# Optimization experiments

Hardware: AMD Instinct MI355X
Metric: run time of the kernel (lower is better)

The kernel has to match this reference:

```python
import jax, jax.numpy as jnp
import numpy as np
from jax import lax

DM, DS, K, EXPAND = 512, 16, 4, 1
DI = EXPAND * DM           # d_inner
DT_RANK = (DM + 15) // 16  # ceil(d_model/16) = 32
B, L = 4, 2048


def setup_inputs() -> dict:
    key = jax.random.key(0)
    ks = jax.random.split(key, 10)
    x = jax.random.normal(ks[0], (B, L, DM), dtype=jnp.float32)
    W_in = jax.random.normal(ks[1], (2 * DI, DM), dtype=jnp.float32) * (1.0 / np.sqrt(DM))
    conv_w = jax.random.normal(ks[2], (DI, 1, K), dtype=jnp.float32) * (1.0 / np.sqrt(K))
    conv_b = jax.random.normal(ks[3], (DI,), dtype=jnp.float32) * 0.02
    W_xproj = jax.random.normal(ks[4], (DT_RANK + 2 * DS, DI), dtype=jnp.float32) * (1.0 / np.sqrt(DI))
    W_dt = jax.random.normal(ks[5], (DI, DT_RANK), dtype=jnp.float32) * (1.0 / np.sqrt(DT_RANK))
    b_dt = jax.random.uniform(ks[6], (DI,), dtype=jnp.float32, minval=-4.0, maxval=-2.0)  # softplus(b)~small dt
    A_log = jnp.log(jnp.broadcast_to(jnp.arange(1, DS + 1, dtype=jnp.float32), (DI, DS)))
    D_param = jnp.ones((DI,), dtype=jnp.float32)
    W_out = jax.random.normal(ks[7], (DM, DI), dtype=jnp.float32) * (1.0 / np.sqrt(DI))
    return {"x": x, "W_in": W_in, "conv_w": conv_w, "conv_b": conv_b,
            "W_xproj": W_xproj, "W_dt": W_dt, "b_dt": b_dt,
            "A_log": A_log, "D_param": D_param, "W_out": W_out}


def _mamba(x, W_in, conv_w, conv_b, W_xproj, W_dt, b_dt, A_log, D_param, W_out):
    # in_proj -> x, z branches [B,L,DI] each
    xz = jnp.einsum('bld,ed->ble', x, W_in)
    xc, z = xz[..., :DI], xz[..., DI:]
    # causal depthwise conv1d over time
    xt = jnp.transpose(xc, (0, 2, 1))                      # [B,DI,L]
    xt = jnp.pad(xt, ((0, 0), (0, 0), (K - 1, 0)))
    xt = lax.conv_general_dilated(xt, conv_w, (1,), 'VALID',
                                  dimension_numbers=('NCH', 'OIH', 'NCH'),
                                  feature_group_count=DI)
    xt = xt + conv_b[None, :, None]
    xc = jax.nn.silu(jnp.transpose(xt, (0, 2, 1)))         # [B,L,DI]
    # input-dependent dt, B, C
    x_dbl = jnp.einsum('bld,ed->ble', xc, W_xproj)         # [B,L,DT_RANK+2*DS]
    dt = x_dbl[..., :DT_RANK]
    Bm = x_dbl[..., DT_RANK:DT_RANK + DS]                  # [B,L,DS]
    Cm = x_dbl[..., DT_RANK + DS:]                         # [B,L,DS]
    dt = jax.nn.softplus(jnp.einsum('blr,dr->bld', dt, W_dt) + b_dt)  # [B,L,DI]
    A = -jnp.exp(A_log)                                    # [DI,DS]
    deltaA = jnp.exp(dt[..., None] * A)                    # [B,L,DI,DS]
    deltaBu = dt[..., None] * Bm[:, :, None, :] * xc[..., None]       # [B,L,DI,DS]

    def step(h, inp):
        dA_t, dBu_t, C_t = inp                             # [B,DI,DS],[B,DI,DS],[B,DS]
        h = dA_t * h + dBu_t
        y = jnp.einsum('bds,bs->bd', h, C_t)
        return h, y

    h0 = jnp.zeros((x.shape[0], DI, DS), dtype=x.dtype)
    _, ys = lax.scan(step, h0, (jnp.transpose(deltaA, (1, 0, 2, 3)),
                                jnp.transpose(deltaBu, (1, 0, 2, 3)),
                                jnp.transpose(Cm, (1, 0, 2))))
    y = jnp.transpose(ys, (1, 0, 2)) + xc * D_param        # [B,L,DI]
    y = y * jax.nn.silu(z)
    out = jnp.einsum('bld,ed->ble', y, W_out)              # [B,L,DM]
    out = jnp.clip(out, -1000.0, 1000.0)
    out = jnp.nan_to_num(out, nan=0.0, posinf=1000.0, neginf=-1000.0)
    return out


def reference(x, W_in, conv_w, conv_b, W_xproj, W_dt, b_dt, A_log, D_param, W_out):
    return _mamba(x, W_in, conv_w, conv_b, W_xproj, W_dt, b_dt, A_log, D_param, W_out)
```

## Files before the change

kernel.cpp:

```cpp
#include <hip/hip_runtime.h>
#include <math.h>

#define DMc   512
#define DIc   512
#define DSc   16
#define KCc   4
#define DTRc  32
#define NXDc  64
#define LLEN  2048
#define BBc   4
#define BLT   (BBc*LLEN)

#define NCH   128
#define CLEN  (LLEN/NCH)

typedef __attribute__((ext_vector_type(8))) short short8;
typedef __attribute__((ext_vector_type(8))) unsigned short ushort8;
typedef __attribute__((ext_vector_type(4))) float f32x4;

__device__ __forceinline__ float sigmoidf_(float x) { return 1.f / (1.f + __expf(-x)); }

__device__ __forceinline__ unsigned short f2bf(float x) {
    unsigned int u = __float_as_uint(x);
    u = (u + 0x7FFFu + ((u >> 16) & 1u)) >> 16;
    return (unsigned short)u;
}

#define CN1 (BLT * DMc / 8)
#define CN2 (1024 * DMc / 8)
#define CN3 (DMc * DIc / 8)
__global__ __launch_bounds__(256) void convert3_kernel(const float* __restrict__ x,
                                                       const float* __restrict__ Win,
                                                       const float* __restrict__ Wout,
                                                       unsigned short* __restrict__ xb,
                                                       unsigned short* __restrict__ Wb,
                                                       unsigned short* __restrict__ Wob)
{
    int i = blockIdx.x * 256 + threadIdx.x;
    const float* src; unsigned short* dst;
    if (i < CN1)                  { src = x;    dst = xb;  }
    else if (i < CN1 + CN2)       { src = Win;  dst = Wb;  i -= CN1; }
    else if (i < CN1 + CN2 + CN3) { src = Wout; dst = Wob; i -= CN1 + CN2; }
    else return;
    float4 a = ((const float4*)src)[2 * i];
    float4 b = ((const float4*)src)[2 * i + 1];
    ushort8 o;
    o[0] = f2bf(a.x); o[1] = f2bf(a.y); o[2] = f2bf(a.z); o[3] = f2bf(a.w);
    o[4] = f2bf(b.x); o[5] = f2bf(b.y); o[6] = f2bf(b.z); o[7] = f2bf(b.w);
    ((ushort8*)dst)[i] = o;
}

template<int EPI>
__global__ __launch_bounds__(256) void gemm_bt_f32(const float* __restrict__ A,
                                                   const float* __restrict__ Bw,
                                                   const float* __restrict__ bias,
                                                   float* __restrict__ C,
                                                   int M, int N, int Kd,
                                                   int lda, int ldb, int ldc)
{
    __shared__ float As[16][68];
    __shared__ float Bs[16][68];
    const int tid  = threadIdx.x;
    const int tx   = tid & 15;
    const int ty   = tid >> 4;
    const int arow = tid >> 2;
    const int akq  = (tid & 3) << 2;

    const float* Ab = A  + (size_t)(blockIdx.y * 64 + arow) * lda + akq;
    const float* Bb = Bw + (size_t)(blockIdx.x * 64 + arow) * ldb + akq;

    float acc[4][4] = {};

    for (int k0 = 0; k0 < Kd; k0 += 16) {
        float4 av = *(const float4*)(Ab + k0);
        float4 bv = *(const float4*)(Bb + k0);
        __syncthreads();
        As[akq + 0][arow] = av.x; As[akq + 1][arow] = av.y;
        As[akq + 2][arow] = av.z; As[akq + 3][arow] = av.w;
        Bs[akq + 0][arow] = bv.x; Bs[akq + 1][arow] = bv.y;
        Bs[akq + 2][arow] = bv.z; Bs[akq + 3][arow] = bv.w;
        __syncthreads();
#pragma unroll
        for (int k = 0; k < 16; ++k) {
            float4 a = *(const float4*)&As[k][ty << 2];
            float4 b = *(const float4*)&Bs[k][tx << 2];
            float ar[4] = {a.x, a.y, a.z, a.w};
            float br[4] = {b.x, b.y, b.z, b.w};
#pragma unroll
            for (int i = 0; i < 4; ++i)
#pragma unroll
                for (int j = 0; j < 4; ++j)
                    acc[i][j] += ar[i] * br[j];
        }
    }

    float4 bv = make_float4(0.f, 0.f, 0.f, 0.f);
    if (EPI == 2) bv = *(const float4*)(bias + blockIdx.x * 64 + (tx << 2));
#pragma unroll
    for (int i = 0; i < 4; ++i) {
        float v[4] = {acc[i][0], acc[i][1], acc[i][2], acc[i][3]};
        if (EPI == 2) {
            float bb[4] = {bv.x, bv.y, bv.z, bv.w};
#pragma unroll
            for (int j = 0; j < 4; ++j) {
                float s = v[j] + bb[j];
                v[j] = fmaxf(s, 0.f) + log1pf(__expf(-fabsf(s)));
            }
        }
        *(float4*)(C + (size_t)(blockIdx.y * 64 + (ty << 2) + i) * ldc
                     + blockIdx.x * 64 + (tx << 2)) = make_float4(v[0], v[1], v[2], v[3]);
    }
}

template<int EPI>
__global__ __launch_bounds__(256) void gemm_mfma(const unsigned short* __restrict__ A,
                                                 const unsigned short* __restrict__ Bw,
                                                 float* __restrict__ C,
                                                 int M, int N, int Kd)
{
    __shared__ short As[128][40];
    __shared__ short Bs[128][40];
    const int tid  = threadIdx.x;
    const int lane = tid & 63;
    const int wv   = tid >> 6;
    const int wr   = wv >> 1;
    const int wc   = wv & 1;
    const int fr   = lane & 15;
    const int fq   = lane >> 4;

    const int rowA0 = blockIdx.y * 128;
    const int rowB0 = blockIdx.x * 128;

    const int r0 = tid >> 2,        s0 = (tid & 3) << 3;
    const int r1 = (tid + 256) >> 2, s1 = s0;

    f32x4 acc[4][4];
#pragma unroll
    for (int m = 0; m < 4; ++m)
#pragma unroll
        for (int n = 0; n < 4; ++n) acc[m][n] = (f32x4){0.f, 0.f, 0.f, 0.f};

    for (int k0 = 0; k0 < Kd; k0 += 32) {
        short8 a0 = *(const short8*)(A  + (size_t)(rowA0 + r0) * Kd + k0 + s0);
        short8 a1 = *(const short8*)(A  + (size_t)(rowA0 + r1) * Kd + k0 + s1);
        short8 b0 = *(const short8*)(Bw + (size_t)(rowB0 + r0) * Kd + k0 + s0);
        short8 b1 = *(const short8*)(Bw + (size_t)(rowB0 + r1) * Kd + k0 + s1);
        __syncthreads();
        *(short8*)&As[r0][s0] = a0;
        *(short8*)&As[r1][s1] = a1;
        *(short8*)&Bs[r0][s0] = b0;
        *(short8*)&Bs[r1][s1] = b1;
        __syncthreads();

        short8 af[4], bf[4];
#pragma unroll
        for (int m = 0; m < 4; ++m)
            af[m] = *(const short8*)&As[wr * 64 + m * 16 + fr][fq << 3];
#pragma unroll
        for (int n = 0; n < 4; ++n)
            bf[n] = *(const short8*)&Bs[wc * 64 + n * 16 + fr][fq << 3];
#pragma unroll
        for (int m = 0; m < 4; ++m)
#pragma unroll
            for (int n = 0; n < 4; ++n)
                acc[m][n] = __builtin_amdgcn_mfma_f32_16x16x32_bf16(af[m], bf[n], acc[m][n], 0, 0, 0);
    }

    const int crow0 = rowA0 + wr * 64 + (fq << 2);
    const int ccol0 = rowB0 + wc * 64 + fr;
#pragma unroll
    for (int m = 0; m < 4; ++m)
#pragma unroll
        for (int n = 0; n < 4; ++n)
#pragma unroll
            for (int j = 0; j < 4; ++j) {
                float v = acc[m][n][j];
                if (EPI) v = (v != v) ? 0.f : fminf(fmaxf(v, -1000.f), 1000.f);
                C[(size_t)(crow0 + m * 16 + j) * N + ccol0 + n * 16] = v;
            }
}

__global__ __launch_bounds__(256) void conv_silu_kernel(const float* __restrict__ xz,
                                                        const float* __restrict__ cw,
                                                        const float* __restrict__ cb,
                                                        float* __restrict__ xc)
{
    int gid = blockIdx.x * 256 + threadIdx.x;
    int d = gid & (DIc - 1);
    int l = (gid >> 9) & (LLEN - 1);
    int b = gid >> 20;
    float s = cb[d];
#pragma unroll
    for (int k = 0; k < KCc; ++k) {
        int ls = l + k - (KCc - 1);
        if (ls >= 0)
            s += xz[((size_t)(b * LLEN + ls) << 10) + d] * cw[d * KCc + k];
    }
    xc[gid] = s * sigmoidf_(s);
}

__device__ __forceinline__ size_t hs_off(int b, int c, int s, int d) {
    return ((size_t)((b * NCH + c) * DSc + s) << 9) + d;
}

__global__ __launch_bounds__(256) void scan_phase1(const float* __restrict__ dtz,
                                                   const float* __restrict__ xc,
                                                   const float* __restrict__ xdbl,
                                                   const float* __restrict__ A_log,
                                                   float* __restrict__ hstate,
                                                   float* __restrict__ sdtbuf)
{
    int half = blockIdx.x & 1;
    int c    = (blockIdx.x >> 1) & (NCH - 1);
    int b    = blockIdx.x >> 8;
    int d    = (half << 8) + threadIdx.x;
    int row0 = b * LLEN + c * CLEN;

    __shared__ float bc[CLEN][32];
    {
        int r = threadIdx.x >> 4, col = (threadIdx.x & 15) << 1;
        const float* src = xdbl + (size_t)(row0 + r) * NXDc + DTRc + col;
        bc[r][col] = src[0]; bc[r][col + 1] = src[1];
    }

    float A[DSc];
#pragma unroll
    for (int s = 0; s < DSc; ++s) A[s] = -__expf(A_log[d * DSc + s]);

    float dtv[CLEN], xcv[CLEN];
#pragma unroll
    for (int t = 0; t < CLEN; ++t) {
        dtv[t] = dtz[((size_t)(row0 + t) << 10) + d];
        xcv[t] = xc [((size_t)(row0 + t) << 9) + d];
    }
    __syncthreads();

    float h[DSc] = {};
    float Sdt = 0.f;
#pragma unroll
    for (int t = 0; t < CLEN; ++t) {
        float dBx = dtv[t] * xcv[t];
        Sdt += dtv[t];
#pragma unroll
        for (int s = 0; s < DSc; ++s)
            h[s] = __expf(dtv[t] * A[s]) * h[s] + dBx * bc[t][s];
    }
#pragma unroll
    for (int s = 0; s < DSc; ++s) hstate[hs_off(b, c, s, d)] = h[s];
    sdtbuf[((size_t)(b * NCH + c) << 9) + d] = Sdt;
}

__global__ __launch_bounds__(64) void scan_phase2(float* __restrict__ hstate,
                                                  const float* __restrict__ sdtbuf,
                                                  const float* __restrict__ A_log)
{
    int gid = blockIdx.x * 64 + threadIdx.x;
    int d = gid & (DIc - 1);
    int s = (gid >> 9) & (DSc - 1);
    int b = gid >> 13;

    float A = -__expf(A_log[d * DSc + s]);
    float h = 0.f;
    for (int c = 0; c < NCH; ++c) {
        size_t o = hs_off(b, c, s, d);
        float he  = hstate[o];
        float Sdt = sdtbuf[((size_t)(b * NCH + c) << 9) + d];
        hstate[o] = h;
        h = __expf(A * Sdt) * h + he;
    }
}

__global__ __launch_bounds__(256) void scan_phase3(const float* __restrict__ dtz,
                                                   const float* __restrict__ xc,
                                                   const float* __restrict__ xdbl,
                                                   const float* __restrict__ hstate,
                                                   const float* __restrict__ A_log,
                                                   const float* __restrict__ Dp,
                                                   unsigned short* __restrict__ yb)
{
    int half = blockIdx.x & 1;
    int c    = (blockIdx.x >> 1) & (NCH - 1);
    int b    = blockIdx.x >> 8;
    int d    = (half << 8) + threadIdx.x;
    int row0 = b * LLEN + c * CLEN;

    __shared__ float bc[CLEN][32];
    {
        int r = threadIdx.x >> 4, col = (threadIdx.x & 15) << 1;
        const float* src = xdbl + (size_t)(row0 + r) * NXDc + DTRc + col;
        bc[r][col] = src[0]; bc[r][col + 1] = src[1];
    }

    float A[DSc];
#pragma unroll
    for (int s = 0; s < DSc; ++s) A[s] = -__expf(A_log[d * DSc + s]);
    float Dv = Dp[d];

    float dtv[CLEN], xcv[CLEN], zv[CLEN];
#pragma unroll
    for (int t = 0; t < CLEN; ++t) {
        dtv[t] = dtz[((size_t)(row0 + t) << 10) + d];
        xcv[t] = xc [((size_t)(row0 + t) << 9) + d];
        zv[t]  = dtz[((size_t)(row0 + t) << 10) + DIc + d];
    }

    float h[DSc];
#pragma unroll
    for (int s = 0; s < DSc; ++s) h[s] = hstate[hs_off(b, c, s, d)];
    __syncthreads();

#pragma unroll
    for (int t = 0; t < CLEN; ++t) {
        float dBx = dtv[t] * xcv[t];
        float acc = 0.f;
#pragma unroll
        for (int s = 0; s < DSc; ++s) {
            float dA = __expf(dtv[t] * A[s]);
            h[s] = dA * h[s] + dBx * bc[t][s];
            acc += h[s] * bc[t][DSc + s];
        }
        float yv = (acc + xcv[t] * Dv) * (zv[t] * sigmoidf_(zv[t]));
        yb[((size_t)(row0 + t) << 9) + d] = f2bf(yv);
    }
}

extern "C" void kernel_launch(void* const* d_in, const int* in_sizes, int n_in,
                              void* d_out, int out_size, void* d_ws, size_t ws_size,
                              hipStream_t stream)
{
    const float* x      = (const float*)d_in[0];
    const float* W_in   = (const float*)d_in[1];
    const float* conv_w = (const float*)d_in[2];
    const float* conv_b = (const float*)d_in[3];
    const float* W_xp   = (const float*)d_in[4];
    const float* W_dt   = (const float*)d_in[5];
    const float* b_dt   = (const float*)d_in[6];
    const float* A_log  = (const float*)d_in[7];
    const float* D_par  = (const float*)d_in[8];
    const float* W_out  = (const float*)d_in[9];
    float* out = (float*)d_out;

    float* ws   = (float*)d_ws;
    float* xz   = ws;
    float* xc   = xz + (size_t)BLT * 1024;
    float* xdbl = xc + (size_t)BLT * DIc;
    unsigned short* xb  = (unsigned short*)(xdbl + (size_t)BLT * NXDc);
    unsigned short* Wb  = xb + (size_t)BLT * DIc;
    unsigned short* Wob = Wb + (size_t)1024 * DMc;
    float* hstate = (float*)(Wob + (size_t)DMc * DIc);
    float* sdtbuf = hstate + (size_t)BBc * NCH * DSc * DIc;

    convert3_kernel<<<(CN1 + CN2 + CN3 + 255) / 256, 256, 0, stream>>>(
        x, W_in, W_out, xb, Wb, Wob);

    gemm_mfma<0><<<dim3(1024 / 128, BLT / 128), 256, 0, stream>>>(xb, Wb, xz, BLT, 1024, DMc);

    conv_silu_kernel<<<(BLT * DIc) / 256, 256, 0, stream>>>(xz, conv_w, conv_b, xc);

    gemm_bt_f32<0><<<dim3(1, BLT / 64), 256, 0, stream>>>(xc, W_xp, nullptr, xdbl,
                                                          BLT, NXDc, DIc, DIc, DIc, NXDc);

    gemm_bt_f32<2><<<dim3(DIc / 64, BLT / 64), 256, 0, stream>>>(xdbl, W_dt, b_dt, xz,
                                                                 BLT, DIc, DTRc, NXDc, DTRc, 1024);

    scan_phase1<<<BBc * NCH * 2, 256, 0, stream>>>(xz, xc, xdbl, A_log, hstate, sdtbuf);
    scan_phase2<<<(BBc * DSc * DIc) / 64, 64, 0, stream>>>(hstate, sdtbuf, A_log);
    scan_phase3<<<BBc * NCH * 2, 256, 0, stream>>>(xz, xc, xdbl, hstate, A_log, D_par, xb);

    gemm_mfma<1><<<dim3(DMc / 128, BLT / 128), 256, 0, stream>>>(xb, Wob, out, BLT, DMc, DMc);
}
```

Before: 169.6 us.

## Store xz and xc intermediates in bf16 and remap GEMM workgroups

The in_proj GEMM now writes bf16 instead of fp32. The conv+SiLU kernel is vectorized to read and write bf16 in groups of 8. The x_proj GEMM gets a dedicated kernel that reads bf16 activations, and the scans read bf16 xc and z with dt kept in a separate compact fp32 buffer. This cuts intermediate memory traffic across several kernels, and a workgroup index swizzle is added to the MFMA GEMM to improve cache locality. The cost is lower precision on activations feeding the SSM scan, which could hurt accuracy.

```diff
diff --git a/kernel.cpp b/kernel.cpp
--- a/kernel.cpp
+++ b/kernel.cpp
@@ -16,6 +16,7 @@
 
 typedef __attribute__((ext_vector_type(8))) short short8;
 typedef __attribute__((ext_vector_type(8))) unsigned short ushort8;
+typedef __attribute__((ext_vector_type(4))) unsigned short bf16x4_t;
 typedef __attribute__((ext_vector_type(4))) float f32x4;
 
 __device__ __forceinline__ float sigmoidf_(float x) { return 1.f / (1.f + __expf(-x)); }
@@ -24,6 +25,9 @@
     unsigned int u = __float_as_uint(x);
     u = (u + 0x7FFFu + ((u >> 16) & 1u)) >> 16;
     return (unsigned short)u;
+}
+__device__ __forceinline__ float bf2f(unsigned short u) {
+    return __uint_as_float((unsigned int)u << 16);
 }
 
 #define CN1 (BLT * DMc / 8)
@@ -112,12 +116,65 @@
     }
 }
 
-template<int EPI>
+__global__ __launch_bounds__(256) void gemm_xdbl(const unsigned short* __restrict__ A,
+                                                 const float* __restrict__ Bw,
+                                                 float* __restrict__ C)
+{
+    __shared__ float As[16][68];
+    __shared__ float Bs[16][68];
+    const int tid  = threadIdx.x;
+    const int tx   = tid & 15;
+    const int ty   = tid >> 4;
+    const int arow = tid >> 2;
+    const int akq  = (tid & 3) << 2;
+
+    const unsigned short* Ab = A + (size_t)(blockIdx.y * 64 + arow) * DIc + akq;
+    const float*          Bb = Bw + (size_t)arow * DIc + akq;
+
+    float acc[4][4] = {};
+
+    for (int k0 = 0; k0 < DIc; k0 += 16) {
+        bf16x4_t av = *(const bf16x4_t*)(Ab + k0);
+        float4   bv = *(const float4*)(Bb + k0);
+        __syncthreads();
+        As[akq + 0][arow] = bf2f(av[0]); As[akq + 1][arow] = bf2f(av[1]);
+        As[akq + 2][arow] = bf2f(av[2]); As[akq + 3][arow] = bf2f(av[3]);
+        Bs[akq + 0][arow] = bv.x; Bs[akq + 1][arow] = bv.y;
+        Bs[akq + 2][arow] = bv.z; Bs[akq + 3][arow] = bv.w;
+        __syncthreads();
+#pragma unroll
+        for (int k = 0; k < 16; ++k) {
+            float4 a = *(const float4*)&As[k][ty << 2];
+            float4 b = *(const float4*)&Bs[k][tx << 2];
+            float ar[4] = {a.x, a.y, a.z, a.w};
+            float br[4] = {b.x, b.y, b.z, b.w};
+#pragma unroll
+            for (int i = 0; i < 4; ++i)
+#pragma unroll
+                for (int j = 0; j < 4; ++j)
+                    acc[i][j] += ar[i] * br[j];
+        }
+    }
+
+#pragma unroll
+    for (int i = 0; i < 4; ++i)
+        *(float4*)(C + (size_t)(blockIdx.y * 64 + (ty << 2) + i) * NXDc + (tx << 2))
+            = make_float4(acc[i][0], acc[i][1], acc[i][2], acc[i][3]);
+}
+
+template<int EPI, int OBF>
 __global__ __launch_bounds__(256) void gemm_mfma(const unsigned short* __restrict__ A,
                                                  const unsigned short* __restrict__ Bw,
-                                                 float* __restrict__ C,
-                                                 int M, int N, int Kd)
-{
+                                                 float* __restrict__ Cf,
+                                                 unsigned short* __restrict__ Cb,
+                                                 int N, int Kd)
+{
+    const int nwg  = gridDim.x * gridDim.y;
+    const int orig = blockIdx.y * gridDim.x + blockIdx.x;
+    const int lg   = (orig & 7) * (nwg >> 3) + (orig >> 3);
+    const int bx   = lg % gridDim.x;
+    const int by   = lg / gridDim.x;
+
     __shared__ short As[128][40];
     __shared__ short Bs[128][40];
     const int tid  = threadIdx.x;
@@ -128,8 +185,8 @@
     const int fr   = lane & 15;
     const int fq   = lane >> 4;
 
-    const int rowA0 = blockIdx.y * 128;
-    const int rowB0 = blockIdx.x * 128;
+    const int rowA0 = by * 128;
+    const int rowB0 = bx * 128;
 
     const int r0 = tid >> 2,        s0 = (tid & 3) << 3;
     const int r1 = (tid + 256) >> 2, s1 = s0;
@@ -176,27 +233,43 @@
             for (int j = 0; j < 4; ++j) {
                 float v = acc[m][n][j];
                 if (EPI) v = (v != v) ? 0.f : fminf(fmaxf(v, -1000.f), 1000.f);
-                C[(size_t)(crow0 + m * 16 + j) * N + ccol0 + n * 16] = v;
+                size_t off = (size_t)(crow0 + m * 16 + j) * N + ccol0 + n * 16;
+                if (OBF) Cb[off] = f2bf(v);
+                else     Cf[off] = v;
             }
 }
 
-__global__ __launch_bounds__(256) void conv_silu_kernel(const float* __restrict__ xz,
+__global__ __launch_bounds__(256) void conv_silu_kernel(const unsigned short* __restrict__ xzb,
                                                         const float* __restrict__ cw,
                                                         const float* __restrict__ cb,
-                                                        float* __restrict__ xc)
+                                                        unsigned short* __restrict__ xcb)
 {
     int gid = blockIdx.x * 256 + threadIdx.x;
-    int d = gid & (DIc - 1);
-    int l = (gid >> 9) & (LLEN - 1);
-    int b = gid >> 20;
-    float s = cb[d];
+    int d8 = gid & 63;
+    int l  = (gid >> 6) & (LLEN - 1);
+    int b  = gid >> 17;
+    int d0 = d8 << 3;
+
+    float s[8];
+#pragma unroll
+    for (int j = 0; j < 8; ++j) s[j] = cb[d0 + j];
 #pragma unroll
     for (int k = 0; k < KCc; ++k) {
         int ls = l + k - (KCc - 1);
-        if (ls >= 0)
-            s += xz[((size_t)(b * LLEN + ls) << 10) + d] * cw[d * KCc + k];
-    }
-    xc[gid] = s * sigmoidf_(s);
+        if (ls >= 0) {
+            ushort8 v = *(const ushort8*)(xzb + (((size_t)(b * LLEN + ls)) << 10) + d0);
+#pragma unroll
+            for (int j = 0; j < 8; ++j)
+                s[j] += bf2f(v[j]) * cw[(d0 + j) * KCc + k];
+        }
+    }
+    ushort8 o;
+#pragma unroll
+    for (int j = 0; j < 8; ++j) {
+        float v = s[j] * sigmoidf_(s[j]);
+        o[j] = f2bf(v);
+    }
+    *(ushort8*)(xcb + ((size_t)gid << 3)) = o;
 }
 
 __device__ __forceinline__ size_t hs_off(int b, int c, int s, int d) {
@@ -204,7 +277,7 @@
 }
 
 __global__ __launch_bounds__(256) void scan_phase1(const float* __restrict__ dtz,
-                                                   const float* __restrict__ xc,
+                                                   const unsigned short* __restrict__ xcb,
                                                    const float* __restrict__ xdbl,
                                                    const float* __restrict__ A_log,
                                                    float* __restrict__ hstate,
@@ -230,8 +303,8 @@
     float dtv[CLEN], xcv[CLEN];
 #pragma unroll
     for (int t = 0; t < CLEN; ++t) {
-        dtv[t] = dtz[((size_t)(row0 + t) << 10) + d];
-        xcv[t] = xc [((size_t)(row0 + t) << 9) + d];
+        dtv[t] = dtz[((size_t)(row0 + t) << 9) + d];
+        xcv[t] = bf2f(xcb[((size_t)(row0 + t) << 9) + d]);
     }
     __syncthreads();
 
@@ -271,8 +344,9 @@
 }
 
 __global__ __launch_bounds__(256) void scan_phase3(const float* __restrict__ dtz,
-                                                   const float* __restrict__ xc,
+                                                   const unsigned short* __restrict__ xcb,
                                                    const float* __restrict__ xdbl,
+                                                   const unsigned short* __restrict__ xzb,
                                                    const float* __restrict__ hstate,
                                                    const float* __restrict__ A_log,
                                                    const float* __restrict__ Dp,
@@ -299,9 +373,9 @@
     float dtv[CLEN], xcv[CLEN], zv[CLEN];
 #pragma unroll
     for (int t = 0; t < CLEN; ++t) {
-        dtv[t] = dtz[((size_t)(row0 + t) << 10) + d];
-        xcv[t] = xc [((size_t)(row0 + t) << 9) + d];
-        zv[t]  = dtz[((size_t)(row0 + t) << 10) + DIc + d];
+        dtv[t] = dtz[((size_t)(row0 + t) << 9) + d];
+        xcv[t] = bf2f(xcb[((size_t)(row0 + t) << 9) + d]);
+        zv[t]  = bf2f(xzb[((size_t)(row0 + t) << 10) + DIc + d]);
     }
 
     float h[DSc];
@@ -340,32 +414,34 @@
     const float* W_out  = (const float*)d_in[9];
     float* out = (float*)d_out;
 
-    float* ws   = (float*)d_ws;
-    float* xz   = ws;
-    float* xc   = xz + (size_t)BLT * 1024;
-    float* xdbl = xc + (size_t)BLT * DIc;
-    unsigned short* xb  = (unsigned short*)(xdbl + (size_t)BLT * NXDc);
-    unsigned short* Wb  = xb + (size_t)BLT * DIc;
-    unsigned short* Wob = Wb + (size_t)1024 * DMc;
-    float* hstate = (float*)(Wob + (size_t)DMc * DIc);
+    unsigned short* xb   = (unsigned short*)d_ws;
+    unsigned short* xzb  = xb  + (size_t)BLT * DIc;
+    unsigned short* xcb  = xzb + (size_t)BLT * 1024;
+    unsigned short* Wb   = xcb + (size_t)BLT * DIc;
+    unsigned short* Wob  = Wb  + (size_t)1024 * DMc;
+    float* xdbl   = (float*)(Wob + (size_t)DMc * DIc);
+    float* dtz    = xdbl + (size_t)BLT * NXDc;
+    float* hstate = dtz  + (size_t)BLT * DIc;
     float* sdtbuf = hstate + (size_t)BBc * NCH * DSc * DIc;
 
     convert3_kernel<<<(CN1 + CN2 + CN3 + 255) / 256, 256, 0, stream>>>(
         x, W_in, W_out, xb, Wb, Wob);
 
-    gemm_mfma<0><<<dim3(1024 / 128, BLT / 128), 256, 0, stream>>>(xb, Wb, xz, BLT, 1024, DMc);
-
-    conv_silu_kernel<<<(BLT * DIc) / 256, 256, 0, stream>>>(xz, conv_w, conv_b, xc);
-
-    gemm_bt_f32<0><<<dim3(1, BLT / 64), 256, 0, stream>>>(xc, W_xp, nullptr, xdbl,
-                                                          BLT, NXDc, DIc, DIc, DIc, NXDc);
-
-    gemm_bt_f32<2><<<dim3(DIc / 64, BLT / 64), 256, 0, stream>>>(xdbl, W_dt, b_dt, xz,
-                                                                 BLT, DIc, DTRc, NXDc, DTRc, 1024);
-
-    scan_phase1<<<BBc * NCH * 2, 256, 0, stream>>>(xz, xc, xdbl, A_log, hstate, sdtbuf);
+    gemm_mfma<0, 1><<<dim3(1024 / 128, BLT / 128), 256, 0, stream>>>(
+        xb, Wb, nullptr, xzb, 1024, DMc);
+
+    conv_silu_kernel<<<(BLT * DIc / 8) / 256, 256, 0, stream>>>(xzb, conv_w, conv_b, xcb);
+
+    gemm_xdbl<<<dim3(1, BLT / 64), 256, 0, stream>>>(xcb, W_xp, xdbl);
+
+    gemm_bt_f32<2><<<dim3(DIc / 64, BLT / 64), 256, 0, stream>>>(
+        xdbl, W_dt, b_dt, dtz, BLT, DIc, DTRc, NXDc, DTRc, DIc);
+
+    scan_phase1<<<BBc * NCH * 2, 256, 0, stream>>>(dtz, xcb, xdbl, A_log, hstate, sdtbuf);
     scan_phase2<<<(BBc * DSc * DIc) / 64, 64, 0, stream>>>(hstate, sdtbuf, A_log);
-    scan_phase3<<<BBc * NCH * 2, 256, 0, stream>>>(xz, xc, xdbl, hstate, A_log, D_par, xb);
-
-    gemm_mfma<1><<<dim3(DMc / 128, BLT / 128), 256, 0, stream>>>(xb, Wob, out, BLT, DMc, DMc);
-}
+    scan_phase3<<<BBc * NCH * 2, 256, 0, stream>>>(dtz, xcb, xdbl, xzb, hstate,
+                                                   A_log, D_par, xb);
+
+    gemm_mfma<1, 0><<<dim3(DMc / 128, BLT / 128), 256, 0, stream>>>(
+        xb, Wob, out, nullptr, DMc, DMc);
+}
```

After: 174.0 us. +2.6%, slower.

## Fuse conv+SiLU into x_proj GEMM and recompute conv in scan kernels

Applied to the files above, without the earlier changes.

Removes the standalone conv/SiLU kernel and the xc intermediate buffer. The x_proj GEMM now computes the causal conv and SiLU on the fly while loading its A tile, and both scan phases recompute xc from xz with the conv weights. dt is written to its own dense buffer instead of overwriting the x half of xz. This saves a launch and a full write and read of xc, at the cost of redundant conv arithmetic and extra xz reads. The x_proj GEMM still runs on only 128 blocks.

```diff
diff --git a/kernel.cpp b/kernel.cpp
--- a/kernel.cpp
+++ b/kernel.cpp
@@ -180,23 +180,72 @@
             }
 }
 
-__global__ __launch_bounds__(256) void conv_silu_kernel(const float* __restrict__ xz,
+__global__ __launch_bounds__(256) void xdbl_conv_kernel(const float* __restrict__ xz,
                                                         const float* __restrict__ cw,
                                                         const float* __restrict__ cb,
-                                                        float* __restrict__ xc)
-{
-    int gid = blockIdx.x * 256 + threadIdx.x;
-    int d = gid & (DIc - 1);
-    int l = (gid >> 9) & (LLEN - 1);
-    int b = gid >> 20;
-    float s = cb[d];
-#pragma unroll
-    for (int k = 0; k < KCc; ++k) {
-        int ls = l + k - (KCc - 1);
-        if (ls >= 0)
-            s += xz[((size_t)(b * LLEN + ls) << 10) + d] * cw[d * KCc + k];
-    }
-    xc[gid] = s * sigmoidf_(s);
+                                                        const float* __restrict__ Wxp,
+                                                        float* __restrict__ xdbl)
+{
+    __shared__ float As[16][68];
+    __shared__ float Bs[16][68];
+    const int tid  = threadIdx.x;
+    const int tx   = tid & 15;
+    const int ty   = tid >> 4;
+    const int arow = tid >> 2;
+    const int akq  = (tid & 3) << 2;
+    const int row0 = blockIdx.y * 64;
+    const int gr   = row0 + arow;
+    const int l    = gr & (LLEN - 1);
+
+    const float* Bb = Wxp + (size_t)arow * DIc + akq;
+
+    float acc[4][4] = {};
+
+    for (int k0 = 0; k0 < DIc; k0 += 16) {
+        const int d0 = k0 + akq;
+        float cwa[4][4];
+#pragma unroll
+        for (int j = 0; j < 4; ++j) {
+            float4 w = *(const float4*)(cw + (size_t)(d0 + j) * KCc);
+            cwa[j][0] = w.x; cwa[j][1] = w.y; cwa[j][2] = w.z; cwa[j][3] = w.w;
+        }
+        float4 cbv = *(const float4*)(cb + d0);
+        float s[4] = {cbv.x, cbv.y, cbv.z, cbv.w};
+#pragma unroll
+        for (int k = 0; k < KCc; ++k) {
+            if (l - (KCc - 1) + k >= 0) {
+                float4 v = *(const float4*)(xz + ((size_t)(gr - (KCc - 1) + k) << 10) + d0);
+                s[0] += v.x * cwa[0][k]; s[1] += v.y * cwa[1][k];
+                s[2] += v.z * cwa[2][k]; s[3] += v.w * cwa[3][k];
+            }
+        }
+        float4 bv = *(const float4*)(Bb + k0);
+        __syncthreads();
+        As[akq + 0][arow] = s[0] * sigmoidf_(s[0]);
+        As[akq + 1][arow] = s[1] * sigmoidf_(s[1]);
+        As[akq + 2][arow] = s[2] * sigmoidf_(s[2]);
+        As[akq + 3][arow] = s[3] * sigmoidf_(s[3]);
+        Bs[akq + 0][arow] = bv.x; Bs[akq + 1][arow] = bv.y;
+        Bs[akq + 2][arow] = bv.z; Bs[akq + 3][arow] = bv.w;
+        __syncthreads();
+#pragma unroll
+        for (int k = 0; k < 16; ++k) {
+            float4 a = *(const float4*)&As[k][ty << 2];
+            float4 b = *(const float4*)&Bs[k][tx << 2];
+            float ar[4] = {a.x, a.y, a.z, a.w};
+            float br[4] = {b.x, b.y, b.z, b.w};
+#pragma unroll
+            for (int i = 0; i < 4; ++i)
+#pragma unroll
+                for (int j = 0; j < 4; ++j)
+                    acc[i][j] += ar[i] * br[j];
+        }
+    }
+
+#pragma unroll
+    for (int i = 0; i < 4; ++i)
+        *(float4*)(xdbl + (size_t)(row0 + (ty << 2) + i) * NXDc + (tx << 2))
+            = make_float4(acc[i][0], acc[i][1], acc[i][2], acc[i][3]);
 }
 
 __device__ __forceinline__ size_t hs_off(int b, int c, int s, int d) {
@@ -204,7 +253,9 @@
 }
 
 __global__ __launch_bounds__(256) void scan_phase1(const float* __restrict__ dtz,
-                                                   const float* __restrict__ xc,
+                                                   const float* __restrict__ xz,
+                                                   const float* __restrict__ cw,
+                                                   const float* __restrict__ cb,
                                                    const float* __restrict__ xdbl,
                                                    const float* __restrict__ A_log,
                                                    float* __restrict__ hstate,
@@ -227,11 +278,22 @@
 #pragma unroll
     for (int s = 0; s < DSc; ++s) A[s] = -__expf(A_log[d * DSc + s]);
 
+    float w0 = cw[d * KCc], w1 = cw[d * KCc + 1], w2 = cw[d * KCc + 2], w3 = cw[d * KCc + 3];
+    float cbv = cb[d];
+    float xv[CLEN + 3];
+#pragma unroll
+    for (int i = 0; i < CLEN + 3; ++i) {
+        xv[i] = (c == 0 && i < 3) ? 0.f
+              : xz[((size_t)(row0 - 3 + i) << 10) + d];
+    }
     float dtv[CLEN], xcv[CLEN];
 #pragma unroll
+    for (int t = 0; t < CLEN; ++t)
+        dtv[t] = dtz[((size_t)(row0 + t) << 9) + d];
+#pragma unroll
     for (int t = 0; t < CLEN; ++t) {
-        dtv[t] = dtz[((size_t)(row0 + t) << 10) + d];
-        xcv[t] = xc [((size_t)(row0 + t) << 9) + d];
+        float s = cbv + xv[t] * w0 + xv[t + 1] * w1 + xv[t + 2] * w2 + xv[t + 3] * w3;
+        xcv[t] = s * sigmoidf_(s);
     }
     __syncthreads();
 
@@ -271,7 +333,9 @@
 }
 
 __global__ __launch_bounds__(256) void scan_phase3(const float* __restrict__ dtz,
-                                                   const float* __restrict__ xc,
+                                                   const float* __restrict__ xz,
+                                                   const float* __restrict__ cw,
+                                                   const float* __restrict__ cb,
                                                    const float* __restrict__ xdbl,
                                                    const float* __restrict__ hstate,
                                                    const float* __restrict__ A_log,
@@ -296,12 +360,24 @@
     for (int s = 0; s < DSc; ++s) A[s] = -__expf(A_log[d * DSc + s]);
     float Dv = Dp[d];
 
+    float w0 = cw[d * KCc], w1 = cw[d * KCc + 1], w2 = cw[d * KCc + 2], w3 = cw[d * KCc + 3];
+    float cbv = cb[d];
+    float xv[CLEN + 3];
+#pragma unroll
+    for (int i = 0; i < CLEN + 3; ++i) {
+        xv[i] = (c == 0 && i < 3) ? 0.f
+              : xz[((size_t)(row0 - 3 + i) << 10) + d];
+    }
     float dtv[CLEN], xcv[CLEN], zv[CLEN];
 #pragma unroll
     for (int t = 0; t < CLEN; ++t) {
-        dtv[t] = dtz[((size_t)(row0 + t) << 10) + d];
-        xcv[t] = xc [((size_t)(row0 + t) << 9) + d];
-        zv[t]  = dtz[((size_t)(row0 + t) << 10) + DIc + d];
+        dtv[t] = dtz[((size_t)(row0 + t) << 9) + d];
+        zv[t]  = xz[((size_t)(row0 + t) << 10) + DIc + d];
+    }
+#pragma unroll
+    for (int t = 0; t < CLEN; ++t) {
+        float s = cbv + xv[t] * w0 + xv[t + 1] * w1 + xv[t + 2] * w2 + xv[t + 3] * w3;
+        xcv[t] = s * sigmoidf_(s);
     }
 
     float h[DSc];
@@ -342,9 +418,9 @@
 
     float* ws   = (float*)d_ws;
     float* xz   = ws;
-    float* xc   = xz + (size_t)BLT * 1024;
-    float* xdbl = xc + (size_t)BLT * DIc;
-    unsigned short* xb  = (unsigned short*)(xdbl + (size_t)BLT * NXDc);
+    float* xdbl = xz + (size_t)BLT * 1024;
+    float* dtz  = xdbl + (size_t)BLT * NXDc;
+    unsigned short* xb  = (unsigned short*)(dtz + (size_t)BLT * DIc);
     unsigned short* Wb  = xb + (size_t)BLT * DIc;
     unsigned short* Wob = Wb + (size_t)1024 * DMc;
     float* hstate = (float*)(Wob + (size_t)DMc * DIc);
@@ -355,17 +431,16 @@
 
     gemm_mfma<0><<<dim3(1024 / 128, BLT / 128), 256, 0, stream>>>(xb, Wb, xz, BLT, 1024, DMc);
 
-    conv_silu_kernel<<<(BLT * DIc) / 256, 256, 0, stream>>>(xz, conv_w, conv_b, xc);
-
-    gemm_bt_f32<0><<<dim3(1, BLT / 64), 256, 0, stream>>>(xc, W_xp, nullptr, xdbl,
-                                                          BLT, NXDc, DIc, DIc, DIc, NXDc);
-
-    gemm_bt_f32<2><<<dim3(DIc / 64, BLT / 64), 256, 0, stream>>>(xdbl, W_dt, b_dt, xz,
-                                                                 BLT, DIc, DTRc, NXDc, DTRc, 1024);
-
-    scan_phase1<<<BBc * NCH * 2, 256, 0, stream>>>(xz, xc, xdbl, A_log, hstate, sdtbuf);
+    xdbl_conv_kernel<<<dim3(1, BLT / 64), 256, 0, stream>>>(xz, conv_w, conv_b, W_xp, xdbl);
+
+    gemm_bt_f32<2><<<dim3(DIc / 64, BLT / 64), 256, 0, stream>>>(xdbl, W_dt, b_dt, dtz,
+                                                                 BLT, DIc, DTRc, NXDc, DTRc, DIc);
+
+    scan_phase1<<<BBc * NCH * 2, 256, 0, stream>>>(dtz, xz, conv_w, conv_b, xdbl,
+                                                   A_log, hstate, sdtbuf);
     scan_phase2<<<(BBc * DSc * DIc) / 64, 64, 0, stream>>>(hstate, sdtbuf, A_log);
-    scan_phase3<<<BBc * NCH * 2, 256, 0, stream>>>(xz, xc, xdbl, hstate, A_log, D_par, xb);
+    scan_phase3<<<BBc * NCH * 2, 256, 0, stream>>>(dtz, xz, conv_w, conv_b, xdbl,
+                                                   hstate, A_log, D_par, xb);
 
     gemm_mfma<1><<<dim3(DMc / 128, BLT / 128), 256, 0, stream>>>(xb, Wob, out, BLT, DMc, DMc);
 }
```

Result: slower. 180.1 us (+6.2%).
